# Optimization experiments

Hardware: AMD Instinct MI355X
Metric: run time of the kernel (lower is better)

## Reference

```python
import math
import jax, jax.numpy as jnp
import numpy as np

K_MODES = 8
L_ITERS = 8
ALPHA_INIT = 2000.0
TAU_INIT = 0.01


def setup_inputs() -> dict:
    key = jax.random.key(0)
    B, T, C = 64, 4096, 16
    x = jax.random.normal(key, (B, T, C), dtype=jnp.float32)
    log_alpha = jnp.full((L_ITERS, K_MODES), math.log(ALPHA_INIT), dtype=jnp.float32)
    raw_tau = jnp.full((L_ITERS,), math.log(math.expm1(TAU_INIT) + 1e-08), dtype=jnp.float32)
    omega_init = np.linspace(0.05, 0.45, K_MODES)
    raw_omega = jnp.asarray(np.log(2.0 * omega_init / (1.0 - 2.0 * omega_init + 1e-08)), dtype=jnp.float32)
    return {"x": x, "log_alpha": log_alpha, "raw_tau": raw_tau, "raw_omega": raw_omega}


def reference(x, log_alpha, raw_tau, raw_omega):
    B, T, C = x.shape
    L, K = log_alpha.shape
    T_rfft = T // 2 + 1

    alpha = jnp.exp(log_alpha)                    # (L, K)
    tau = jax.nn.softplus(raw_tau)                # (L,)
    omega = jax.nn.sigmoid(raw_omega) * 0.5       # (K,)

    freqs = jnp.linspace(0.0, 0.5, T_rfft, dtype=x.dtype)  # (T_rfft,)
    # (B, T, C) -> (B*C, T)
    x_bc = jnp.transpose(x, (0, 2, 1)).reshape(B * C, T)
    f_hat = jnp.fft.rfft(x_bc, axis=-1)           # (B*C, T_rfft) complex

    # Precompute all denominators: (L, K, T_rfft)
    denom = 1.0 + 2.0 * alpha[:, :, None] * (freqs[None, None, :] - omega[None, :, None]) ** 2

    u0 = jnp.zeros((B * C, K, T_rfft), dtype=f_hat.dtype)
    lam0 = jnp.zeros_like(f_hat)

    def step(carry, per_layer):
        u, lam = carry
        den_l, tau_l = per_layer
        u_sum = u.sum(axis=1)  # (B*C, T_rfft)
        # Jacobi update for all K modes simultaneously
        numerator = f_hat[:, None, :] - (u_sum[:, None, :] - u) + 0.5 * lam[:, None, :]
        u_new = numerator / den_l[None, :, :]
        lam_new = lam + tau_l * (f_hat - u_new.sum(axis=1))
        return (u_new, lam_new), None

    (u_final, _), _ = jax.lax.scan(step, (u0, lam0), (denom, tau))

    modes_flat = jnp.fft.irfft(u_final, n=T, axis=-1)  # (B*C, K, T)
    modes = jnp.transpose(modes_flat.reshape(B, C, K, T), (0, 2, 3, 1))  # (B, K, T, C)
    return modes
```

## Files before the change

### kernel.cpp

```cpp
#include <hip/hip_runtime.h>
#include <math.h>

#ifndef M_PI
#define M_PI 3.14159265358979323846
#endif

#define T_LEN 4096
#define M_LEN 2048
#define NFREQ 2049
#define KM 8
#define LI 8
#define CD 16

template <int NT>
__device__ __forceinline__ float2* fft2048(float2* a, float2* b, int tid, float sign) {
    float2* src = a;
    float2* dst = b;
    int l = 1024;
    #pragma unroll 1
    for (int s = 0; s < 11; ++s) {
        float piol = sign * (float)M_PI / (float)l;
        #pragma unroll
        for (int ii = 0; ii < 1024 / NT; ++ii) {
            int i = tid + ii * NT;
            int j = i >> s;
            float2 A = src[i];
            float2 B = src[i + 1024];
            float ang = piol * (float)j;
            float sw, cw;
            __sincosf(ang, &sw, &cw);
            float2 sum = make_float2(A.x + B.x, A.y + B.y);
            float2 dif = make_float2(A.x - B.x, A.y - B.y);
            float2 tw = make_float2(dif.x * cw - dif.y * sw, dif.x * sw + dif.y * cw);
            int p = i + (j << s);
            dst[p] = sum;
            dst[p + (1 << s)] = tw;
        }
        __syncthreads();
        float2* t = src; src = dst; dst = t;
        l >>= 1;
    }
    return src;
}

__global__ void __launch_bounds__(512)
k_fwd_iter(const float* __restrict__ x,
           const float* __restrict__ log_alpha,
           const float* __restrict__ raw_tau,
           const float* __restrict__ raw_omega,
           float2* __restrict__ u_ws)
{
    __shared__ float2 bufA[M_LEN];
    __shared__ float2 bufB[M_LEN];
    __shared__ float s_2a[LI * KM];
    __shared__ float s_tau[LI];
    __shared__ float s_om[KM];

    const int tid = threadIdx.x;
    const int row = blockIdx.x;
    const int b = row >> 4;
    const int c = row & 15;

    if (tid < LI * KM) s_2a[tid] = 2.0f * __expf(log_alpha[tid]);
    if (tid < LI)      s_tau[tid] = log1pf(__expf(raw_tau[tid]));
    if (tid < KM)      s_om[tid]  = 0.5f / (1.0f + __expf(-raw_omega[tid]));

    const float* xr = x + (size_t)b * T_LEN * CD + c;
    #pragma unroll
    for (int q = 0; q < 4; ++q) {
        int n = tid + q * 512;
        float e = xr[(size_t)(2 * n) * CD];
        float o = xr[(size_t)(2 * n + 1) * CD];
        bufA[n] = make_float2(e, o);
    }
    __syncthreads();

    float2* Z = fft2048<512>(bufA, bufB, tid, -1.0f);

    const size_t sb = (size_t)(b * (KM * CD) + c);

    for (int f = tid; f < NFREQ; f += 512) {
        float2 Zk = Z[f & (M_LEN - 1)];
        float2 Zm = Z[(M_LEN - f) & (M_LEN - 1)];
        float2 E = make_float2(0.5f * (Zk.x + Zm.x), 0.5f * (Zk.y - Zm.y));
        float2 D = make_float2(0.5f * (Zk.x - Zm.x), 0.5f * (Zk.y + Zm.y));
        float2 O = make_float2(D.y, -D.x);
        float ang = -2.0f * (float)M_PI * (float)f / (float)T_LEN;
        float sw, cw;
        __sincosf(ang, &sw, &cw);
        float fhx = E.x + cw * O.x - sw * O.y;
        float fhy = E.y + cw * O.y + sw * O.x;

        float freq = (float)f * (0.5f / (float)M_LEN);
        float dd[KM];
        #pragma unroll
        for (int k = 0; k < KM; ++k) {
            float d = freq - s_om[k];
            dd[k] = d * d;
        }

        float2 u[KM];
        #pragma unroll
        for (int k = 0; k < KM; ++k) u[k] = make_float2(0.f, 0.f);
        float lamx = 0.f, lamy = 0.f;

        #pragma unroll
        for (int l = 0; l < LI; ++l) {
            float usx = 0.f, usy = 0.f;
            #pragma unroll
            for (int k = 0; k < KM; ++k) { usx += u[k].x; usy += u[k].y; }
            float bx = fhx - usx + 0.5f * lamx;
            float by = fhy - usy + 0.5f * lamy;
            float sx = 0.f, sy = 0.f;
            #pragma unroll
            for (int k = 0; k < KM; ++k) {
                float den = fmaf(s_2a[l * KM + k], dd[k], 1.0f);
                float r = __builtin_amdgcn_rcpf(den);
                float ux = (bx + u[k].x) * r;
                float uy = (by + u[k].y) * r;
                u[k].x = ux; u[k].y = uy;
                sx += ux; sy += uy;
            }
            lamx += s_tau[l] * (fhx - sx);
            lamy += s_tau[l] * (fhy - sy);
        }

        #pragma unroll
        for (int k = 0; k < KM; ++k) {
            u_ws[(sb + (size_t)k * CD) * NFREQ + f] = u[k];
        }
    }
}

__global__ void __launch_bounds__(1024)
k_inv(const float2* __restrict__ u_ws, float* __restrict__ out)
{
    __shared__ float2 bufA[NFREQ];
    __shared__ float2 bufB[M_LEN];
    const int tid = threadIdx.x;
    const int bk = blockIdx.x;

    float val[CD][4];

    #pragma unroll
    for (int c = 0; c < CD; ++c) {
        const float2* sp = u_ws + (size_t)(bk * CD + c) * NFREQ;
        bufA[tid] = sp[tid];
        bufA[tid + 1024] = sp[tid + 1024];
        if (tid == 0) bufA[2048] = sp[2048];
        __syncthreads();

        #pragma unroll
        for (int jj = 0; jj < 2; ++jj) {
            int j = tid + jj * 1024;
            float2 Xj = bufA[j];
            float2 Xm = bufA[M_LEN - j];
            float2 E = make_float2(0.5f * (Xj.x + Xm.x), 0.5f * (Xj.y - Xm.y));
            float2 D = make_float2(0.5f * (Xj.x - Xm.x), 0.5f * (Xj.y + Xm.y));
            float ang = 2.0f * (float)M_PI * (float)j / (float)T_LEN;
            float sw, cw;
            __sincosf(ang, &sw, &cw);
            float2 O = make_float2(cw * D.x - sw * D.y, cw * D.y + sw * D.x);
            const float sc = 1.0f / (float)M_LEN;
            bufB[j] = make_float2((E.x - O.y) * sc, (E.y + O.x) * sc);
        }
        __syncthreads();

        float2* res = fft2048<1024>(bufB, bufA, tid, 1.0f);
        float2 z0 = res[2 * tid];
        float2 z1 = res[2 * tid + 1];
        val[c][0] = z0.x;
        val[c][1] = z0.y;
        val[c][2] = z1.x;
        val[c][3] = z1.y;
        __syncthreads();
    }

    float4* op = (float4*)(out + ((size_t)bk * T_LEN + (size_t)(4 * tid)) * CD);
    #pragma unroll
    for (int r = 0; r < 4; ++r) {
        #pragma unroll
        for (int g = 0; g < 4; ++g) {
            op[r * 4 + g] = make_float4(val[4 * g + 0][r], val[4 * g + 1][r],
                                        val[4 * g + 2][r], val[4 * g + 3][r]);
        }
    }
}

extern "C" void kernel_launch(void* const* d_in, const int* in_sizes, int n_in,
                              void* d_out, int out_size, void* d_ws, size_t ws_size,
                              hipStream_t stream) {
    const float* x         = (const float*)d_in[0];
    const float* log_alpha = (const float*)d_in[1];
    const float* raw_tau   = (const float*)d_in[2];
    const float* raw_omega = (const float*)d_in[3];
    float* out = (float*)d_out;
    float2* u_ws = (float2*)d_ws;

    k_fwd_iter<<<dim3(64 * CD), dim3(512), 0, stream>>>(x, log_alpha, raw_tau,
                                                        raw_omega, u_ws);
    k_inv<<<dim3(64 * KM), dim3(1024), 0, stream>>>(u_ws, out);
}
```

Baseline: 397.0 us.

## Replace radix-2 shared-memory FFT with padded in-place radix-8 FFT passes

```diff
diff --git a/kernel.cpp b/kernel.cpp
--- a/kernel.cpp
+++ b/kernel.cpp
@@ -1,120 +1,145 @@
 #include <hip/hip_runtime.h>
 #include <math.h>
 
-#ifndef M_PI
-#define M_PI 3.14159265358979323846
-#endif
-
-#define T_LEN 4096
-#define M_LEN 2048
-#define NFREQ 2049
-#define KM 8
-#define LI 8
-#define CD 16
-
-template <int NT>
-__device__ __forceinline__ float2* fft2048(float2* a, float2* b, int tid, float sign) {
-    float2* src = a;
-    float2* dst = b;
-    int l = 1024;
-    #pragma unroll 1
-    for (int s = 0; s < 11; ++s) {
-        float piol = sign * (float)M_PI / (float)l;
-        #pragma unroll
-        for (int ii = 0; ii < 1024 / NT; ++ii) {
-            int i = tid + ii * NT;
-            int j = i >> s;
-            float2 A = src[i];
-            float2 B = src[i + 1024];
-            float ang = piol * (float)j;
-            float sw, cw;
-            __sincosf(ang, &sw, &cw);
-            float2 sum = make_float2(A.x + B.x, A.y + B.y);
-            float2 dif = make_float2(A.x - B.x, A.y - B.y);
-            float2 tw = make_float2(dif.x * cw - dif.y * sw, dif.x * sw + dif.y * cw);
-            int p = i + (j << s);
-            dst[p] = sum;
-            dst[p + (1 << s)] = tw;
-        }
-        __syncthreads();
-        float2* t = src; src = dst; dst = t;
-        l >>= 1;
-    }
-    return src;
-}
-
-__global__ void __launch_bounds__(512)
-k_fwd_iter(const float* __restrict__ x,
-           const float* __restrict__ log_alpha,
-           const float* __restrict__ raw_tau,
-           const float* __restrict__ raw_omega,
-           float2* __restrict__ u_ws)
+#define TWO_PI 6.283185307179586f
+#define C_SQ2 0.70710678118654752f
+#define FSTR 2049
+
+__device__ __forceinline__ int PH(int i) { return i + (i >> 3); }
+
+__device__ __forceinline__ float2 cadd(float2 a, float2 b){ return make_float2(a.x+b.x, a.y+b.y); }
+__device__ __forceinline__ float2 csub(float2 a, float2 b){ return make_float2(a.x-b.x, a.y-b.y); }
+__device__ __forceinline__ float2 cmul(float2 a, float2 b){ return make_float2(a.x*b.x - a.y*b.y, a.x*b.y + a.y*b.x); }
+
+template<int SGN>
+__device__ __forceinline__ float2 cmulj(float2 a){
+    return (SGN > 0) ? make_float2(-a.y, a.x) : make_float2(a.y, -a.x);
+}
+
+template<int SGN>
+__device__ __forceinline__ void dft4(float2 a0, float2 a1, float2 a2, float2 a3,
+                                     float2& y0, float2& y1, float2& y2, float2& y3) {
+    float2 s0 = cadd(a0, a2), d0 = csub(a0, a2);
+    float2 s1 = cadd(a1, a3), d1 = cmulj<SGN>(csub(a1, a3));
+    y0 = cadd(s0, s1); y1 = cadd(d0, d1); y2 = csub(s0, s1); y3 = csub(d0, d1);
+}
+
+template<int SGN>
+__device__ __forceinline__ void dft8(const float2 x[8], float2 y[8]) {
+    float2 E0,E1,E2,E3,O0,O1,O2,O3;
+    dft4<SGN>(x[0],x[2],x[4],x[6],E0,E1,E2,E3);
+    dft4<SGN>(x[1],x[3],x[5],x[7],O0,O1,O2,O3);
+    const float sg = (float)SGN;
+    float2 t1 = make_float2(C_SQ2*(O1.x - sg*O1.y), C_SQ2*(O1.y + sg*O1.x));
+    float2 t2 = cmulj<SGN>(O2);
+    float2 t3 = make_float2(-C_SQ2*(O3.x + sg*O3.y), C_SQ2*(sg*O3.x - O3.y));
+    y[0]=cadd(E0,O0); y[4]=csub(E0,O0);
+    y[1]=cadd(E1,t1); y[5]=csub(E1,t1);
+    y[2]=cadd(E2,t2); y[6]=csub(E2,t2);
+    y[3]=cadd(E3,t3); y[7]=csub(E3,t3);
+}
+
+template<int SGN, int P>
+__device__ __forceinline__ void fft_pass(float2* buf, int st) {
+    float2 v[8], y[8];
+    #pragma unroll
+    for (int r = 0; r < 8; ++r) v[r] = buf[PH(st + 256*r)];
+    dft8<SGN>(v, y);
+    const int m = 1 << (3*P);
+    const int j = st >> (3*P);
+    const int q = st & (m-1);
+    float th = (float)SGN * (TWO_PI / (float)(2048 >> (3*P))) * (float)j;
+    float sw, cw; __sincosf(th, &sw, &cw);
+    float2 w1 = make_float2(cw, sw);
+    float2 w2 = cmul(w1,w1), w3 = cmul(w1,w2), w4 = cmul(w2,w2),
+           w5 = cmul(w2,w3), w6 = cmul(w3,w3), w7 = cmul(w3,w4);
+    y[1]=cmul(y[1],w1); y[2]=cmul(y[2],w2); y[3]=cmul(y[3],w3);
+    y[4]=cmul(y[4],w4); y[5]=cmul(y[5],w5); y[6]=cmul(y[6],w6); y[7]=cmul(y[7],w7);
+    __syncthreads();
+    const int base = q + 8*m*j;
+    #pragma unroll
+    for (int r = 0; r < 8; ++r) buf[PH(base + r*m)] = y[r];
+    __syncthreads();
+}
+
+template<int SGN>
+__device__ __forceinline__ void fft_last(const float2* buf, int st, float2 out[8]) {
+    #pragma unroll
+    for (int h = 0; h < 2; ++h) {
+        int q = st + 256*h;
+        float2 y0,y1,y2,y3;
+        dft4<SGN>(buf[PH(q)], buf[PH(q+512)], buf[PH(q+1024)], buf[PH(q+1536)],
+                  y0, y1, y2, y3);
+        out[0*2+h] = y0; out[1*2+h] = y1; out[2*2+h] = y2; out[3*2+h] = y3;
+    }
+}
+
+__global__ void __launch_bounds__(256)
+k_fwd(const float* __restrict__ x, const float* __restrict__ log_alpha,
+      const float* __restrict__ raw_tau, const float* __restrict__ raw_omega,
+      float2* __restrict__ u_ws)
 {
-    __shared__ float2 bufA[M_LEN];
-    __shared__ float2 bufB[M_LEN];
-    __shared__ float s_2a[LI * KM];
-    __shared__ float s_tau[LI];
-    __shared__ float s_om[KM];
-
-    const int tid = threadIdx.x;
-    const int row = blockIdx.x;
-    const int b = row >> 4;
-    const int c = row & 15;
-
-    if (tid < LI * KM) s_2a[tid] = 2.0f * __expf(log_alpha[tid]);
-    if (tid < LI)      s_tau[tid] = log1pf(__expf(raw_tau[tid]));
-    if (tid < KM)      s_om[tid]  = 0.5f / (1.0f + __expf(-raw_omega[tid]));
-
-    const float* xr = x + (size_t)b * T_LEN * CD + c;
-    #pragma unroll
-    for (int q = 0; q < 4; ++q) {
-        int n = tid + q * 512;
-        float e = xr[(size_t)(2 * n) * CD];
-        float o = xr[(size_t)(2 * n + 1) * CD];
-        bufA[n] = make_float2(e, o);
-    }
-    __syncthreads();
-
-    float2* Z = fft2048<512>(bufA, bufB, tid, -1.0f);
-
-    const size_t sb = (size_t)(b * (KM * CD) + c);
-
-    for (int f = tid; f < NFREQ; f += 512) {
-        float2 Zk = Z[f & (M_LEN - 1)];
-        float2 Zm = Z[(M_LEN - f) & (M_LEN - 1)];
-        float2 E = make_float2(0.5f * (Zk.x + Zm.x), 0.5f * (Zk.y - Zm.y));
-        float2 D = make_float2(0.5f * (Zk.x - Zm.x), 0.5f * (Zk.y + Zm.y));
+    __shared__ float2 buf[2304];
+    __shared__ float s_2a[64], s_tau[8], s_om[8];
+    const int st = threadIdx.x;
+    const int b = blockIdx.x >> 4, c = blockIdx.x & 15;
+
+    if (st < 64) s_2a[st] = 2.0f * __expf(log_alpha[st]);
+    if (st < 8)  s_tau[st] = log1pf(__expf(raw_tau[st]));
+    if (st < 8)  s_om[st]  = 0.5f / (1.0f + __expf(-raw_omega[st]));
+
+    const float* xr = x + (size_t)b * 4096 * 16 + c;
+    #pragma unroll
+    for (int i = 0; i < 8; ++i) {
+        int n = st + 256*i;
+        float e = xr[(size_t)(2*n)   * 16];
+        float o = xr[(size_t)(2*n+1) * 16];
+        buf[PH(n)] = make_float2(e, o);
+    }
+    __syncthreads();
+
+    fft_pass<-1,0>(buf, st);
+    fft_pass<-1,1>(buf, st);
+    fft_pass<-1,2>(buf, st);
+    float2 zz[8];
+    fft_last<-1>(buf, st, zz);
+    #pragma unroll
+    for (int i = 0; i < 8; ++i) buf[PH(st + 256*i)] = zz[i];
+    __syncthreads();
+
+    const size_t sb = (size_t)(b*128 + c);
+    for (int f = st; f < 2049; f += 256) {
+        float2 Zk = buf[PH(f & 2047)];
+        float2 Zm = buf[PH((2048 - f) & 2047)];
+        float2 E = make_float2(0.5f*(Zk.x+Zm.x), 0.5f*(Zk.y-Zm.y));
+        float2 D = make_float2(0.5f*(Zk.x-Zm.x), 0.5f*(Zk.y+Zm.y));
         float2 O = make_float2(D.y, -D.x);
-        float ang = -2.0f * (float)M_PI * (float)f / (float)T_LEN;
-        float sw, cw;
-        __sincosf(ang, &sw, &cw);
-        float fhx = E.x + cw * O.x - sw * O.y;
-        float fhy = E.y + cw * O.y + sw * O.x;
-
-        float freq = (float)f * (0.5f / (float)M_LEN);
-        float dd[KM];
-        #pragma unroll
-        for (int k = 0; k < KM; ++k) {
-            float d = freq - s_om[k];
-            dd[k] = d * d;
-        }
-
-        float2 u[KM];
-        #pragma unroll
-        for (int k = 0; k < KM; ++k) u[k] = make_float2(0.f, 0.f);
+        float ang = -(TWO_PI/4096.f) * (float)f;
+        float sw, cw; __sincosf(ang, &sw, &cw);
+        float fhx = E.x + cw*O.x - sw*O.y;
+        float fhy = E.y + cw*O.y + sw*O.x;
+
+        float freq = (float)f * (0.5f/2048.f);
+        float dd[8];
+        #pragma unroll
+        for (int k = 0; k < 8; ++k) { float d = freq - s_om[k]; dd[k] = d*d; }
+
+        float2 u[8];
+        #pragma unroll
+        for (int k = 0; k < 8; ++k) u[k] = make_float2(0.f, 0.f);
         float lamx = 0.f, lamy = 0.f;
 
         #pragma unroll
-        for (int l = 0; l < LI; ++l) {
+        for (int l = 0; l < 8; ++l) {
             float usx = 0.f, usy = 0.f;
             #pragma unroll
-            for (int k = 0; k < KM; ++k) { usx += u[k].x; usy += u[k].y; }
-            float bx = fhx - usx + 0.5f * lamx;
-            float by = fhy - usy + 0.5f * lamy;
+            for (int k = 0; k < 8; ++k) { usx += u[k].x; usy += u[k].y; }
+            float bx = fhx - usx + 0.5f*lamx;
+            float by = fhy - usy + 0.5f*lamy;
             float sx = 0.f, sy = 0.f;
             #pragma unroll
-            for (int k = 0; k < KM; ++k) {
-                float den = fmaf(s_2a[l * KM + k], dd[k], 1.0f);
+            for (int k = 0; k < 8; ++k) {
+                float den = fmaf(s_2a[l*8+k], dd[k], 1.0f);
                 float r = __builtin_amdgcn_rcpf(den);
                 float ux = (bx + u[k].x) * r;
                 float uy = (by + u[k].y) * r;
@@ -126,64 +151,65 @@
         }
 
         #pragma unroll
-        for (int k = 0; k < KM; ++k) {
-            u_ws[(sb + (size_t)k * CD) * NFREQ + f] = u[k];
-        }
+        for (int k = 0; k < 8; ++k)
+            u_ws[(sb + (size_t)k*16) * FSTR + f] = u[k];
     }
 }
 
 __global__ void __launch_bounds__(1024)
 k_inv(const float2* __restrict__ u_ws, float* __restrict__ out)
 {
-    __shared__ float2 bufA[NFREQ];
-    __shared__ float2 bufB[M_LEN];
+    __shared__ float2 lds[4][2304];
     const int tid = threadIdx.x;
+    const int sg = tid >> 8, st = tid & 255;
     const int bk = blockIdx.x;
-
-    float val[CD][4];
-
-    #pragma unroll
-    for (int c = 0; c < CD; ++c) {
-        const float2* sp = u_ws + (size_t)(bk * CD + c) * NFREQ;
-        bufA[tid] = sp[tid];
-        bufA[tid + 1024] = sp[tid + 1024];
-        if (tid == 0) bufA[2048] = sp[2048];
-        __syncthreads();
-
-        #pragma unroll
-        for (int jj = 0; jj < 2; ++jj) {
-            int j = tid + jj * 1024;
-            float2 Xj = bufA[j];
-            float2 Xm = bufA[M_LEN - j];
-            float2 E = make_float2(0.5f * (Xj.x + Xm.x), 0.5f * (Xj.y - Xm.y));
-            float2 D = make_float2(0.5f * (Xj.x - Xm.x), 0.5f * (Xj.y + Xm.y));
-            float ang = 2.0f * (float)M_PI * (float)j / (float)T_LEN;
-            float sw, cw;
-            __sincosf(ang, &sw, &cw);
-            float2 O = make_float2(cw * D.x - sw * D.y, cw * D.y + sw * D.x);
-            const float sc = 1.0f / (float)M_LEN;
-            bufB[j] = make_float2((E.x - O.y) * sc, (E.y + O.x) * sc);
+    float2* buf = lds[sg];
+
+    float2 val[4][8];
+
+    #pragma unroll
+    for (int ci = 0; ci < 4; ++ci) {
+        const int cc = 4*sg + ci;
+        const float2* sp = u_ws + (size_t)(bk*16 + cc) * FSTR;
+        #pragma unroll
+        for (int i = 0; i < 8; ++i) buf[PH(st + 256*i)] = sp[st + 256*i];
+        if (st == 0) buf[2303] = sp[2048];
+        __syncthreads();
+
+        float2 zreg[8];
+        #pragma unroll
+        for (int i = 0; i < 8; ++i) {
+            int j2 = st + 256*i;
+            float2 Xj = buf[PH(j2)];
+            float2 Xm = (j2 == 0) ? buf[2303] : buf[PH(2048 - j2)];
+            float2 E = make_float2(0.5f*(Xj.x+Xm.x), 0.5f*(Xj.y-Xm.y));
+            float2 D = make_float2(0.5f*(Xj.x-Xm.x), 0.5f*(Xj.y+Xm.y));
+            float ang = (TWO_PI/4096.f) * (float)j2;
+            float sw, cw; __sincosf(ang, &sw, &cw);
+            float2 O = make_float2(cw*D.x - sw*D.y, cw*D.y + sw*D.x);
+            const float sc = 1.0f/2048.f;
+            zreg[i] = make_float2((E.x - O.y)*sc, (E.y + O.x)*sc);
         }
         __syncthreads();
-
-        float2* res = fft2048<1024>(bufB, bufA, tid, 1.0f);
-        float2 z0 = res[2 * tid];
-        float2 z1 = res[2 * tid + 1];
-        val[c][0] = z0.x;
-        val[c][1] = z0.y;
-        val[c][2] = z1.x;
-        val[c][3] = z1.y;
-        __syncthreads();
-    }
-
-    float4* op = (float4*)(out + ((size_t)bk * T_LEN + (size_t)(4 * tid)) * CD);
-    #pragma unroll
-    for (int r = 0; r < 4; ++r) {
-        #pragma unroll
-        for (int g = 0; g < 4; ++g) {
-            op[r * 4 + g] = make_float4(val[4 * g + 0][r], val[4 * g + 1][r],
-                                        val[4 * g + 2][r], val[4 * g + 3][r]);
-        }
+        #pragma unroll
+        for (int i = 0; i < 8; ++i) buf[PH(st + 256*i)] = zreg[i];
+        __syncthreads();
+
+        fft_pass<1,0>(buf, st);
+        fft_pass<1,1>(buf, st);
+        fft_pass<1,2>(buf, st);
+        fft_last<1>(buf, st, val[ci]);
+        __syncthreads();
+    }
+
+    const size_t ob = (size_t)bk * 4096 * 16;
+    #pragma unroll
+    for (int i = 0; i < 8; ++i) {
+        int n = st + 256*i;
+        float4 A = make_float4(val[0][i].x, val[1][i].x, val[2][i].x, val[3][i].x);
+        float4 B = make_float4(val[0][i].y, val[1][i].y, val[2][i].y, val[3][i].y);
+        *(float4*)(out + ob + (size_t)(2*n)  *16 + 4*sg) = A;
+        *(float4*)(out + ob + (size_t)(2*n+1)*16 + 4*sg) = B;
     }
 }
 
@@ -197,7 +223,6 @@
     float* out = (float*)d_out;
     float2* u_ws = (float2*)d_ws;
 
-    k_fwd_iter<<<dim3(64 * CD), dim3(512), 0, stream>>>(x, log_alpha, raw_tau,
-                                                        raw_omega, u_ws);
-    k_inv<<<dim3(64 * KM), dim3(1024), 0, stream>>>(u_ws, out);
-}
+    k_fwd<<<dim3(1024), dim3(256), 0, stream>>>(x, log_alpha, raw_tau, raw_omega, u_ws);
+    k_inv<<<dim3(512), dim3(1024), 0, stream>>>(u_ws, out);
+}
```

Result: slower. 461.9 us (+16.3%).
